# Kernel optimization log

Hardware: AMD Instinct MI355X
Metric: run time of the kernel (lower is better)

Reference implementation:

```python
import jax, jax.numpy as jnp
import numpy as np

T_STEPS = 4
HIDDEN = 2048
INTER = 5504
BSZ = 2
SEQ = 512


def setup_inputs() -> dict:
    key = jax.random.key(0)
    k1, k2, k3, k4 = jax.random.split(key, 4)
    scale_h = 1.0 / np.sqrt(HIDDEN)
    scale_i = 1.0 / np.sqrt(INTER)
    return {
        "x": jax.random.normal(k1, (T_STEPS * BSZ, SEQ, HIDDEN), dtype=jnp.float32),
        "w_gate": jax.random.normal(k2, (INTER, HIDDEN), dtype=jnp.float32) * scale_h,
        "w_up": jax.random.normal(k3, (INTER, HIDDEN), dtype=jnp.float32) * scale_h,
        "w_down": jax.random.normal(k4, (HIDDEN, INTER), dtype=jnp.float32) * scale_i,
        "T": T_STEPS,
    }


def reference(x, w_gate, w_up, w_down, T):
    BT, D, L = x.shape
    bsz = BT // T
    xt = x.reshape(T, bsz, D, L)  # (T, bsz, seq, hidden)

    # gate/up projections per timestep
    out_g = jnp.einsum("tbsh,ih->tbsi", xt, w_gate)   # (T, bsz, seq, inter)
    out_up = jnp.einsum("tbsh,ih->tbsi", xt, w_up)

    # Sequential membrane accumulation: X_t = sum_{k<=t} out_g[k], Y_t = silu(X_t),
    # A_t = Y_t - Y_{t-1} (Y_{-1} = 0)
    Y = jax.nn.silu(jnp.cumsum(out_g, axis=0))
    A = jnp.concatenate([Y[:1], Y[1:] - Y[:-1]], axis=0)  # act_out_g

    # compute_hadamard_v2 collapses in closed form:
    # C[m] = A[m]*B[m] + 0.5*sum_{j!=m}(A[m]*B[j] + A[j]*B[m])
    #      = 0.5*(A[m]*sum(B) + B[m]*sum(A))
    SA = jnp.sum(A, axis=0)       # (bsz, seq, inter)
    SB = jnp.sum(out_up, axis=0)
    C = 0.5 * (A * SB[None] + out_up * SA[None])  # (T, bsz, seq, inter)

    down = jnp.einsum("tbsi,hi->tbsh", C, w_down)  # (T, bsz, seq, hidden)
    return down.reshape(BT, D, L)
```

## Files before the change

kernel.cpp:

```cpp
#include <hip/hip_runtime.h>
#include <cstdint>
#include <cstddef>

#define HIDDEN 2048
#define INTER 5504
#define BS_ROWS 1024
#define MROWS 4096

typedef short bf16x8 __attribute__((ext_vector_type(8)));
typedef float f32x4 __attribute__((ext_vector_type(4)));

#define WAIT_VMCNT(N) asm volatile("s_waitcnt vmcnt(" #N ")" ::: "memory")

__device__ __forceinline__ void barrier_raw() {
  asm volatile("" ::: "memory");
  __builtin_amdgcn_s_barrier();
  asm volatile("" ::: "memory");
}

__device__ __forceinline__ unsigned short f2bf(float f) {
  unsigned int u = __float_as_uint(f);
  u += 0x7fffu + ((u >> 16) & 1u);
  return (unsigned short)(u >> 16);
}

__global__ void convert_kernel(const float* __restrict__ in,
                               unsigned short* __restrict__ out, int n4) {
  int i = blockIdx.x * blockDim.x + threadIdx.x;
  if (i >= n4) return;
  float4 v = reinterpret_cast<const float4*>(in)[i];
  ushort4 o;
  o.x = f2bf(v.x); o.y = f2bf(v.y); o.z = f2bf(v.z); o.w = f2bf(v.w);
  reinterpret_cast<ushort4*>(out)[i] = o;
}

__device__ __forceinline__ void gload16(const unsigned short* g, unsigned short* lds) {
  __builtin_amdgcn_global_load_lds(
      (const __attribute__((address_space(1))) unsigned int*)g,
      (__attribute__((address_space(3))) unsigned int*)lds, 16, 0, 0);
}


__global__ __launch_bounds__(512, 2) void gemm1_fused(
    const unsigned short* __restrict__ xb,
    const unsigned short* __restrict__ wg,
    const unsigned short* __restrict__ wu,
    unsigned short* __restrict__ cb) {
  extern __shared__ unsigned short smem[];
  unsigned short* Abuf = smem;
  unsigned short* Gbuf = smem + 2 * 16384;
  unsigned short* Ubuf = smem + 2 * 16384 + 2 * 8192;

  const int tid = threadIdx.x;
  const int lane = tid & 63;
  const int wv = tid >> 6;
  const int wr = wv >> 1;
  const int wc = wv & 1;

  const int lin = blockIdx.x * 16 + blockIdx.y;
  const int swz = (lin & 7) * 86 + (lin >> 3);
  const int bx = swz / 16, by = swz % 16;
  const int r0 = by * 64;
  const int n0 = bx * 128;

  const int l3 = lane >> 3;
  const int sslot = (((lane & 7) ^ l3) * 8);

  f32x4 accg[4][4], accu[4][4];
#pragma unroll
  for (int m = 0; m < 4; ++m)
#pragma unroll
    for (int n = 0; n < 4; ++n) {
      accg[m][n] = f32x4{0.f, 0.f, 0.f, 0.f};
      accu[m][n] = f32x4{0.f, 0.f, 0.f, 0.f};
    }

  auto STAGE = [&](int k0, int b) {
    unsigned short* Ad = Abuf + b * 16384;
    unsigned short* Gd = Gbuf + b * 8192;
    unsigned short* Ud = Ubuf + b * 8192;
#pragma unroll
    for (int c = 0; c < 4; ++c) {
      const int idx = c * 8 + wv;
      const int row = idx * 8 + l3;
      const int t = (row >> 4) & 3;
      const int grow = t * BS_ROWS + r0 + (row >> 6) * 16 + (row & 15);
      gload16(xb + (size_t)grow * HIDDEN + k0 + sslot, Ad + idx * 512);
    }
#pragma unroll
    for (int c = 0; c < 2; ++c) {
      const int idx = c * 8 + wv;
      const int row = idx * 8 + l3;
      gload16(wg + (size_t)(n0 + row) * HIDDEN + k0 + sslot, Gd + idx * 512);
      gload16(wu + (size_t)(n0 + row) * HIDDEN + k0 + sslot, Ud + idx * 512);
    }
  };

  const int NT = HIDDEN / 64;
  STAGE(0, 0);
  STAGE(64, 1);

  const int m15 = lane & 15;
  const int kbase = (lane >> 4) * 8;
  const int rsw = (lane & 7) * 8;
  int cur = 0;

  for (int t = 0; t < NT; ++t) {
    if (t + 1 < NT) { WAIT_VMCNT(8); } else { WAIT_VMCNT(0); }
    barrier_raw();
    const unsigned short* Ar = Abuf + cur * 16384;
    const unsigned short* Gr = Gbuf + cur * 8192;
    const unsigned short* Ur = Ubuf + cur * 8192;
#pragma unroll
    for (int kk = 0; kk < 2; ++kk) {
      const int col = (kk * 32 + kbase) ^ rsw;
      bf16x8 af[4], bgf[4], buf[4];
#pragma unroll
      for (int m = 0; m < 4; ++m)
        af[m] = *reinterpret_cast<const bf16x8*>(Ar + (wr * 64 + m * 16 + m15) * 64 + col);
#pragma unroll
      for (int n = 0; n < 4; ++n) {
        const int row = wc * 64 + n * 16 + m15;
        bgf[n] = *reinterpret_cast<const bf16x8*>(Gr + row * 64 + col);
        buf[n] = *reinterpret_cast<const bf16x8*>(Ur + row * 64 + col);
      }
      __builtin_amdgcn_s_setprio(1);
#pragma unroll
      for (int m = 0; m < 4; ++m)
#pragma unroll
        for (int n = 0; n < 4; ++n) {
          accg[m][n] = __builtin_amdgcn_mfma_f32_16x16x32_bf16(af[m], bgf[n], accg[m][n], 0, 0, 0);
          accu[m][n] = __builtin_amdgcn_mfma_f32_16x16x32_bf16(af[m], buf[n], accu[m][n], 0, 0, 0);
        }
      __builtin_amdgcn_s_setprio(0);
    }
    barrier_raw();
    if (t + 2 < NT) STAGE((t + 2) * 64, cur);
    cur ^= 1;
  }

  const int cc = lane & 15;
  const int jj0 = (lane >> 4) * 4;
#pragma unroll
  for (int n = 0; n < 4; ++n) {
    const int col = n0 + wc * 64 + n * 16 + cc;
#pragma unroll
    for (int r = 0; r < 4; ++r) {
      const int row_bs = r0 + wr * 16 + jj0 + r;
      const float g0 = accg[0][n][r], g1 = accg[1][n][r];
      const float g2 = accg[2][n][r], g3 = accg[3][n][r];
      const float u0 = accu[0][n][r], u1 = accu[1][n][r];
      const float u2 = accu[2][n][r], u3 = accu[3][n][r];
      float xx = g0;
      const float y0 = xx / (1.f + __expf(-xx));
      xx += g1;
      const float y1 = xx / (1.f + __expf(-xx));
      xx += g2;
      const float y2 = xx / (1.f + __expf(-xx));
      xx += g3;
      const float y3 = xx / (1.f + __expf(-xx));
      const float sa = y3;
      const float sb = u0 + u1 + u2 + u3;
      const size_t base = (size_t)row_bs * INTER + col;
      const size_t ts = (size_t)BS_ROWS * INTER;
      cb[base]          = f2bf(0.5f * (y0 * sb + u0 * sa));
      cb[base + ts]     = f2bf(0.5f * ((y1 - y0) * sb + u1 * sa));
      cb[base + 2 * ts] = f2bf(0.5f * ((y2 - y1) * sb + u2 * sa));
      cb[base + 3 * ts] = f2bf(0.5f * ((y3 - y2) * sb + u3 * sa));
    }
  }
}

__global__ __launch_bounds__(512, 2) void gemm2_down(
    const unsigned short* __restrict__ cb,
    const unsigned short* __restrict__ wd,
    float* __restrict__ out) {
  extern __shared__ unsigned short smem[];
  unsigned short* Abuf = smem;
  unsigned short* Bbuf = smem + 2 * 16384;

  const int tid = threadIdx.x;
  const int lane = tid & 63;
  const int wv = tid >> 6;
  const int wr = wv >> 1;
  const int wc = wv & 1;

  const int lin = blockIdx.x * 16 + blockIdx.y;
  const int swz = (lin & 7) * 32 + (lin >> 3);
  const int bx = swz / 16, by = swz % 16;
  const int m0 = by * 256;
  const int n0 = bx * 128;

  const int l3 = lane >> 3;
  const int sslot = (((lane & 7) ^ l3) * 8);

  f32x4 acc[4][4];
#pragma unroll
  for (int m = 0; m < 4; ++m)
#pragma unroll
    for (int n = 0; n < 4; ++n) acc[m][n] = f32x4{0.f, 0.f, 0.f, 0.f};

  auto STAGE = [&](int k0, int b) {
    unsigned short* Ad = Abuf + b * 16384;
    unsigned short* Bd = Bbuf + b * 8192;
#pragma unroll
    for (int c = 0; c < 4; ++c) {
      const int idx = c * 8 + wv;
      const int row = idx * 8 + l3;
      gload16(cb + (size_t)(m0 + row) * INTER + k0 + sslot, Ad + idx * 512);
    }
#pragma unroll
    for (int c = 0; c < 2; ++c) {
      const int idx = c * 8 + wv;
      const int row = idx * 8 + l3;
      gload16(wd + (size_t)(n0 + row) * INTER + k0 + sslot, Bd + idx * 512);
    }
  };

  const int NT = INTER / 64;
  STAGE(0, 0);
  STAGE(64, 1);

  const int m15 = lane & 15;
  const int kbase = (lane >> 4) * 8;
  const int rsw = (lane & 7) * 8;
  int cur = 0;

  for (int t = 0; t < NT; ++t) {
    if (t + 1 < NT) { WAIT_VMCNT(6); } else { WAIT_VMCNT(0); }
    barrier_raw();
    const unsigned short* Ar = Abuf + cur * 16384;
    const unsigned short* Br = Bbuf + cur * 8192;
#pragma unroll
    for (int kk = 0; kk < 2; ++kk) {
      const int col = (kk * 32 + kbase) ^ rsw;
      bf16x8 af[4], bf[4];
#pragma unroll
      for (int m = 0; m < 4; ++m)
        af[m] = *reinterpret_cast<const bf16x8*>(Ar + (wr * 64 + m * 16 + m15) * 64 + col);
#pragma unroll
      for (int n = 0; n < 4; ++n)
        bf[n] = *reinterpret_cast<const bf16x8*>(Br + (wc * 64 + n * 16 + m15) * 64 + col);
      __builtin_amdgcn_s_setprio(1);
#pragma unroll
      for (int m = 0; m < 4; ++m)
#pragma unroll
        for (int n = 0; n < 4; ++n)
          acc[m][n] = __builtin_amdgcn_mfma_f32_16x16x32_bf16(af[m], bf[n], acc[m][n], 0, 0, 0);
      __builtin_amdgcn_s_setprio(0);
    }
    barrier_raw();
    if (t + 2 < NT) STAGE((t + 2) * 64, cur);
    cur ^= 1;
  }

  const int cc = lane & 15;
  const int jj0 = (lane >> 4) * 4;
#pragma unroll
  for (int m = 0; m < 4; ++m)
#pragma unroll
    for (int n = 0; n < 4; ++n)
#pragma unroll
      for (int r = 0; r < 4; ++r)
        out[(size_t)(m0 + wr * 64 + m * 16 + jj0 + r) * HIDDEN +
            n0 + wc * 64 + n * 16 + cc] = acc[m][n][r];
}

extern "C" void kernel_launch(void* const* d_in, const int* in_sizes, int n_in,
                              void* d_out, int out_size, void* d_ws, size_t ws_size,
                              hipStream_t stream) {
  (void)in_sizes; (void)n_in; (void)out_size;
  const size_t need_elems = (size_t)MROWS * HIDDEN + 3 * (size_t)INTER * HIDDEN +
                            (size_t)MROWS * INTER;
  if (ws_size < need_elems * sizeof(unsigned short)) return;

  const float* x = (const float*)d_in[0];
  const float* w_gate = (const float*)d_in[1];
  const float* w_up = (const float*)d_in[2];
  const float* w_down = (const float*)d_in[3];
  float* out = (float*)d_out;

  unsigned short* xb = (unsigned short*)d_ws;
  unsigned short* wgb = xb + (size_t)MROWS * HIDDEN;
  unsigned short* wub = wgb + (size_t)INTER * HIDDEN;
  unsigned short* wdb = wub + (size_t)INTER * HIDDEN;
  unsigned short* cb = wdb + (size_t)INTER * HIDDEN;

  (void)hipFuncSetAttribute(reinterpret_cast<const void*>(gemm1_fused),
                            hipFuncAttributeMaxDynamicSharedMemorySize, 131072);
  (void)hipFuncSetAttribute(reinterpret_cast<const void*>(gemm2_down),
                            hipFuncAttributeMaxDynamicSharedMemorySize, 98304);

  {
    int n4 = MROWS * HIDDEN / 4;
    convert_kernel<<<(n4 + 255) / 256, 256, 0, stream>>>(x, xb, n4);
  }
  {
    int n4 = INTER * HIDDEN / 4;
    convert_kernel<<<(n4 + 255) / 256, 256, 0, stream>>>(w_gate, wgb, n4);
    convert_kernel<<<(n4 + 255) / 256, 256, 0, stream>>>(w_up, wub, n4);
    convert_kernel<<<(n4 + 255) / 256, 256, 0, stream>>>(w_down, wdb, n4);
  }

  gemm1_fused<<<dim3(INTER / 128, BS_ROWS / 64), 512, 131072, stream>>>(xb, wgb, wub, cb);
  gemm2_down<<<dim3(HIDDEN / 128, MROWS / 256), 512, 98304, stream>>>(cb, wdb, out);
}
```

Measured before the change: 469.6 us.

## Interleave LDS reads and MFMA phases with barriers; triple-buffer down GEMM

Both GEMM main loops are split into phases: LDS fragment loads, then a barrier, then an MFMA cluster, so waves take turns between memory and matrix work in a ping-pong style. The down-projection kernel moves from double to triple buffering with prefetch distance three, which raises its shared memory to 144KB. The goal is to hide LDS and global load latency behind MFMA. The cost is extra barriers per iteration, and the larger LDS footprint may cut gemm2 occupancy below the two blocks per CU its launch bounds assume.

New measurement: 472.2 us. About the same (+0.6%).

```diff
diff --git a/kernel.cpp b/kernel.cpp
--- a/kernel.cpp
+++ b/kernel.cpp
@@ -11,6 +11,7 @@
 typedef float f32x4 __attribute__((ext_vector_type(4)));
 
 #define WAIT_VMCNT(N) asm volatile("s_waitcnt vmcnt(" #N ")" ::: "memory")
+#define WAIT_LGKM0()  asm volatile("s_waitcnt lgkmcnt(0)" ::: "memory")
 
 __device__ __forceinline__ void barrier_raw() {
   asm volatile("" ::: "memory");
@@ -106,36 +107,79 @@
   int cur = 0;
 
   for (int t = 0; t < NT; ++t) {
-    if (t + 1 < NT) { WAIT_VMCNT(8); } else { WAIT_VMCNT(0); }
+    if (t < NT - 1) { WAIT_VMCNT(8); } else { WAIT_VMCNT(0); }
     barrier_raw();
     const unsigned short* Ar = Abuf + cur * 16384;
     const unsigned short* Gr = Gbuf + cur * 8192;
     const unsigned short* Ur = Ubuf + cur * 8192;
-#pragma unroll
-    for (int kk = 0; kk < 2; ++kk) {
-      const int col = (kk * 32 + kbase) ^ rsw;
-      bf16x8 af[4], bgf[4], buf[4];
-#pragma unroll
-      for (int m = 0; m < 4; ++m)
-        af[m] = *reinterpret_cast<const bf16x8*>(Ar + (wr * 64 + m * 16 + m15) * 64 + col);
-#pragma unroll
-      for (int n = 0; n < 4; ++n) {
-        const int row = wc * 64 + n * 16 + m15;
-        bgf[n] = *reinterpret_cast<const bf16x8*>(Gr + row * 64 + col);
-        buf[n] = *reinterpret_cast<const bf16x8*>(Ur + row * 64 + col);
-      }
-      __builtin_amdgcn_s_setprio(1);
-#pragma unroll
-      for (int m = 0; m < 4; ++m)
-#pragma unroll
-        for (int n = 0; n < 4; ++n) {
-          accg[m][n] = __builtin_amdgcn_mfma_f32_16x16x32_bf16(af[m], bgf[n], accg[m][n], 0, 0, 0);
-          accu[m][n] = __builtin_amdgcn_mfma_f32_16x16x32_bf16(af[m], buf[n], accu[m][n], 0, 0, 0);
-        }
-      __builtin_amdgcn_s_setprio(0);
-    }
+    const int colk0 = kbase ^ rsw;
+    const int colk1 = (32 + kbase) ^ rsw;
+
+    bf16x8 a0[4], g0[4];
+#pragma unroll
+    for (int m = 0; m < 4; ++m)
+      a0[m] = *reinterpret_cast<const bf16x8*>(Ar + (wr * 64 + m * 16 + m15) * 64 + colk0);
+#pragma unroll
+    for (int n = 0; n < 4; ++n)
+      g0[n] = *reinterpret_cast<const bf16x8*>(Gr + (wc * 64 + n * 16 + m15) * 64 + colk0);
+    barrier_raw();
+    WAIT_LGKM0();
+    __builtin_amdgcn_s_setprio(1);
+#pragma unroll
+    for (int m = 0; m < 4; ++m)
+#pragma unroll
+      for (int n = 0; n < 4; ++n)
+        accg[m][n] = __builtin_amdgcn_mfma_f32_16x16x32_bf16(a0[m], g0[n], accg[m][n], 0, 0, 0);
+    __builtin_amdgcn_s_setprio(0);
+    barrier_raw();
+
+    bf16x8 u0[4];
+#pragma unroll
+    for (int n = 0; n < 4; ++n)
+      u0[n] = *reinterpret_cast<const bf16x8*>(Ur + (wc * 64 + n * 16 + m15) * 64 + colk0);
+    barrier_raw();
+    WAIT_LGKM0();
+    __builtin_amdgcn_s_setprio(1);
+#pragma unroll
+    for (int m = 0; m < 4; ++m)
+#pragma unroll
+      for (int n = 0; n < 4; ++n)
+        accu[m][n] = __builtin_amdgcn_mfma_f32_16x16x32_bf16(a0[m], u0[n], accu[m][n], 0, 0, 0);
+    __builtin_amdgcn_s_setprio(0);
+    barrier_raw();
+
+    bf16x8 a1[4], g1[4];
+#pragma unroll
+    for (int m = 0; m < 4; ++m)
+      a1[m] = *reinterpret_cast<const bf16x8*>(Ar + (wr * 64 + m * 16 + m15) * 64 + colk1);
+#pragma unroll
+    for (int n = 0; n < 4; ++n)
+      g1[n] = *reinterpret_cast<const bf16x8*>(Gr + (wc * 64 + n * 16 + m15) * 64 + colk1);
+    barrier_raw();
+    WAIT_LGKM0();
+    __builtin_amdgcn_s_setprio(1);
+#pragma unroll
+    for (int m = 0; m < 4; ++m)
+#pragma unroll
+      for (int n = 0; n < 4; ++n)
+        accg[m][n] = __builtin_amdgcn_mfma_f32_16x16x32_bf16(a1[m], g1[n], accg[m][n], 0, 0, 0);
+    __builtin_amdgcn_s_setprio(0);
+    barrier_raw();
+
+    bf16x8 u1[4];
+#pragma unroll
+    for (int n = 0; n < 4; ++n)
+      u1[n] = *reinterpret_cast<const bf16x8*>(Ur + (wc * 64 + n * 16 + m15) * 64 + colk1);
     barrier_raw();
     if (t + 2 < NT) STAGE((t + 2) * 64, cur);
+    WAIT_LGKM0();
+    __builtin_amdgcn_s_setprio(1);
+#pragma unroll
+    for (int m = 0; m < 4; ++m)
+#pragma unroll
+      for (int n = 0; n < 4; ++n)
+        accu[m][n] = __builtin_amdgcn_mfma_f32_16x16x32_bf16(a1[m], u1[n], accu[m][n], 0, 0, 0);
+    __builtin_amdgcn_s_setprio(0);
     cur ^= 1;
   }
 
@@ -147,26 +191,26 @@
 #pragma unroll
     for (int r = 0; r < 4; ++r) {
       const int row_bs = r0 + wr * 16 + jj0 + r;
-      const float g0 = accg[0][n][r], g1 = accg[1][n][r];
-      const float g2 = accg[2][n][r], g3 = accg[3][n][r];
-      const float u0 = accu[0][n][r], u1 = accu[1][n][r];
-      const float u2 = accu[2][n][r], u3 = accu[3][n][r];
-      float xx = g0;
+      const float g0_ = accg[0][n][r], g1_ = accg[1][n][r];
+      const float g2_ = accg[2][n][r], g3_ = accg[3][n][r];
+      const float u0_ = accu[0][n][r], u1_ = accu[1][n][r];
+      const float u2_ = accu[2][n][r], u3_ = accu[3][n][r];
+      float xx = g0_;
       const float y0 = xx / (1.f + __expf(-xx));
-      xx += g1;
+      xx += g1_;
       const float y1 = xx / (1.f + __expf(-xx));
-      xx += g2;
+      xx += g2_;
       const float y2 = xx / (1.f + __expf(-xx));
-      xx += g3;
+      xx += g3_;
       const float y3 = xx / (1.f + __expf(-xx));
       const float sa = y3;
-      const float sb = u0 + u1 + u2 + u3;
+      const float sb = u0_ + u1_ + u2_ + u3_;
       const size_t base = (size_t)row_bs * INTER + col;
       const size_t ts = (size_t)BS_ROWS * INTER;
-      cb[base]          = f2bf(0.5f * (y0 * sb + u0 * sa));
-      cb[base + ts]     = f2bf(0.5f * ((y1 - y0) * sb + u1 * sa));
-      cb[base + 2 * ts] = f2bf(0.5f * ((y2 - y1) * sb + u2 * sa));
-      cb[base + 3 * ts] = f2bf(0.5f * ((y3 - y2) * sb + u3 * sa));
+      cb[base]          = f2bf(0.5f * (y0 * sb + u0_ * sa));
+      cb[base + ts]     = f2bf(0.5f * ((y1 - y0) * sb + u1_ * sa));
+      cb[base + 2 * ts] = f2bf(0.5f * ((y2 - y1) * sb + u2_ * sa));
+      cb[base + 3 * ts] = f2bf(0.5f * ((y3 - y2) * sb + u3_ * sa));
     }
   }
 }
@@ -177,7 +221,7 @@
     float* __restrict__ out) {
   extern __shared__ unsigned short smem[];
   unsigned short* Abuf = smem;
-  unsigned short* Bbuf = smem + 2 * 16384;
+  unsigned short* Bbuf = smem + 3 * 16384;
 
   const int tid = threadIdx.x;
   const int lane = tid & 63;
@@ -220,6 +264,7 @@
   const int NT = INTER / 64;
   STAGE(0, 0);
   STAGE(64, 1);
+  STAGE(128, 2);
 
   const int m15 = lane & 15;
   const int kbase = (lane >> 4) * 8;
@@ -227,31 +272,51 @@
   int cur = 0;
 
   for (int t = 0; t < NT; ++t) {
-    if (t + 1 < NT) { WAIT_VMCNT(6); } else { WAIT_VMCNT(0); }
+    if (t < NT - 2) { WAIT_VMCNT(12); }
+    else if (t == NT - 2) { WAIT_VMCNT(6); }
+    else { WAIT_VMCNT(0); }
     barrier_raw();
     const unsigned short* Ar = Abuf + cur * 16384;
     const unsigned short* Br = Bbuf + cur * 8192;
-#pragma unroll
-    for (int kk = 0; kk < 2; ++kk) {
-      const int col = (kk * 32 + kbase) ^ rsw;
-      bf16x8 af[4], bf[4];
-#pragma unroll
-      for (int m = 0; m < 4; ++m)
-        af[m] = *reinterpret_cast<const bf16x8*>(Ar + (wr * 64 + m * 16 + m15) * 64 + col);
-#pragma unroll
-      for (int n = 0; n < 4; ++n)
-        bf[n] = *reinterpret_cast<const bf16x8*>(Br + (wc * 64 + n * 16 + m15) * 64 + col);
-      __builtin_amdgcn_s_setprio(1);
-#pragma unroll
-      for (int m = 0; m < 4; ++m)
-#pragma unroll
-        for (int n = 0; n < 4; ++n)
-          acc[m][n] = __builtin_amdgcn_mfma_f32_16x16x32_bf16(af[m], bf[n], acc[m][n], 0, 0, 0);
-      __builtin_amdgcn_s_setprio(0);
-    }
-    barrier_raw();
-    if (t + 2 < NT) STAGE((t + 2) * 64, cur);
-    cur ^= 1;
+    const int colk0 = kbase ^ rsw;
+    const int colk1 = (32 + kbase) ^ rsw;
+
+    bf16x8 a0[4], b0[4];
+#pragma unroll
+    for (int m = 0; m < 4; ++m)
+      a0[m] = *reinterpret_cast<const bf16x8*>(Ar + (wr * 64 + m * 16 + m15) * 64 + colk0);
+#pragma unroll
+    for (int n = 0; n < 4; ++n)
+      b0[n] = *reinterpret_cast<const bf16x8*>(Br + (wc * 64 + n * 16 + m15) * 64 + colk0);
+    barrier_raw();
+    WAIT_LGKM0();
+    __builtin_amdgcn_s_setprio(1);
+#pragma unroll
+    for (int m = 0; m < 4; ++m)
+#pragma unroll
+      for (int n = 0; n < 4; ++n)
+        acc[m][n] = __builtin_amdgcn_mfma_f32_16x16x32_bf16(a0[m], b0[n], acc[m][n], 0, 0, 0);
+    __builtin_amdgcn_s_setprio(0);
+    barrier_raw();
+
+    bf16x8 a1[4], b1[4];
+#pragma unroll
+    for (int m = 0; m < 4; ++m)
+      a1[m] = *reinterpret_cast<const bf16x8*>(Ar + (wr * 64 + m * 16 + m15) * 64 + colk1);
+#pragma unroll
+    for (int n = 0; n < 4; ++n)
+      b1[n] = *reinterpret_cast<const bf16x8*>(Br + (wc * 64 + n * 16 + m15) * 64 + colk1);
+    barrier_raw();
+    if (t + 3 < NT) STAGE((t + 3) * 64, cur);
+    WAIT_LGKM0();
+    __builtin_amdgcn_s_setprio(1);
+#pragma unroll
+    for (int m = 0; m < 4; ++m)
+#pragma unroll
+      for (int n = 0; n < 4; ++n)
+        acc[m][n] = __builtin_amdgcn_mfma_f32_16x16x32_bf16(a1[m], b1[n], acc[m][n], 0, 0, 0);
+    __builtin_amdgcn_s_setprio(0);
+    cur = (cur + 1) % 3;
   }
 
   const int cc = lane & 15;
@@ -289,7 +354,7 @@
   (void)hipFuncSetAttribute(reinterpret_cast<const void*>(gemm1_fused),
                             hipFuncAttributeMaxDynamicSharedMemorySize, 131072);
   (void)hipFuncSetAttribute(reinterpret_cast<const void*>(gemm2_down),
-                            hipFuncAttributeMaxDynamicSharedMemorySize, 98304);
+                            hipFuncAttributeMaxDynamicSharedMemorySize, 147456);
 
   {
     int n4 = MROWS * HIDDEN / 4;
@@ -303,5 +368,5 @@
   }
 
   gemm1_fused<<<dim3(INTER / 128, BS_ROWS / 64), 512, 131072, stream>>>(xb, wgb, wub, cb);
-  gemm2_down<<<dim3(HIDDEN / 128, MROWS / 256), 512, 98304, stream>>>(cb, wdb, out);
-}
+  gemm2_down<<<dim3(HIDDEN / 128, MROWS / 256), 512, 147456, stream>>>(cb, wdb, out);
+}
```
